# Kernel optimization log

Measured on AMD Instinct MI355X. Metric: run time of the kernel, lower is better.

Reference implementation:

```python
import jax, jax.numpy as jnp
import numpy as np

BN_EPS = 1e-5

def _conv(x, w, bias=None):
    # x: [N,C,H,W], w: [O,I,3,3], SAME padding, stride 1
    y = jax.lax.conv_general_dilated(x, w, window_strides=(1, 1),
                                     padding=((1, 1), (1, 1)),
                                     dimension_numbers=('NCHW', 'OIHW', 'NCHW'))
    if bias is not None:
        y = y + bias[None, :, None, None]
    return y

def _cconv(xr, xi, wr, wi):
    # complex conv: (xr + i xi) * (wr + i wi), cross-term combination
    return _conv(xr, wr) - _conv(xi, wi), _conv(xr, wi) + _conv(xi, wr)

def _bn1(x, g, b):
    # per-channel batchnorm (training-style stats over N,H,W)
    mu = jnp.mean(x, axis=(0, 2, 3), keepdims=True)
    var = jnp.var(x, axis=(0, 2, 3), keepdims=True)
    xh = (x - mu) * jax.lax.rsqrt(var + BN_EPS)
    return xh * g[None, :, None, None] + b[None, :, None, None]

def _cbn(xr, xi, g, b):
    # naive complex BN: normalize real/imag parts separately, shared affine
    return _bn1(xr, g, b), _bn1(xi, g, b)

def _crelu(xr, xi):
    return jax.nn.relu(xr), jax.nn.relu(xi)

def setup_inputs() -> dict:
    key = jax.random.key(0)
    ks = jax.random.split(key, 16)
    def w(k, o, i, kh=3, kw=3, s=0.05):
        return jax.random.normal(k, (o, i, kh, kw), jnp.float32) * s
    d = {}
    d['x'] = jax.random.normal(ks[0], (4, 256, 128, 224), jnp.float32)
    d['w1r'] = w(ks[1], 144, 256); d['w1i'] = w(ks[2], 144, 256)
    d['g1'] = jnp.ones((144,), jnp.float32); d['b1'] = jnp.zeros((144,), jnp.float32)
    d['w2r'] = w(ks[3], 96, 144); d['w2i'] = w(ks[4], 96, 144)
    d['g2'] = jnp.ones((96,), jnp.float32); d['b2'] = jnp.zeros((96,), jnp.float32)
    d['w3r'] = w(ks[5], 96, 96); d['w3i'] = w(ks[6], 96, 96)
    d['g3'] = jnp.ones((96,), jnp.float32); d['b3'] = jnp.zeros((96,), jnp.float32)
    d['w4r'] = w(ks[7], 96, 96); d['w4i'] = w(ks[8], 96, 96)
    d['g4'] = jnp.ones((96,), jnp.float32); d['b4'] = jnp.zeros((96,), jnp.float32)
    d['wc'] = w(ks[9], 1, 96); d['bc'] = jnp.zeros((1,), jnp.float32)
    d['wg'] = w(ks[10], 2, 96); d['bg'] = jnp.zeros((2,), jnp.float32)
    return d

def reference(x, w1r, w1i, g1, b1, w2r, w2i, g2, b2,
              w3r, w3i, g3, b3, w4r, w4i, g4, b4, wc, bc, wg, bg):
    # real input promoted to complex with zero imag
    xr, xi = x, jnp.zeros_like(x)
    xr, xi = _cconv(xr, xi, w1r, w1i)
    xr, xi = _cbn(xr, xi, g1, b1)
    xr, xi = _crelu(xr, xi)
    xr, xi = _cconv(xr, xi, w2r, w2i)
    xr, xi = _cbn(xr, xi, g2, b2)
    xr, xi = _crelu(xr, xi)
    xr, xi = _cconv(xr, xi, w3r, w3i)
    xr, xi = _cbn(xr, xi, g3, b3)
    xr, xi = _crelu(xr, xi)
    xr, xi = _cconv(xr, xi, w4r, w4i)
    xr, xi = _cbn(xr, xi, g4, b4)
    xr, xi = _crelu(xr, xi)
    x_mag = jnp.sqrt(xr * xr + xi * xi)  # torch.abs on complex
    cls = jax.nn.sigmoid(_conv(x_mag, wc, bc))
    reg = _conv(x_mag, wg, bg)
    return jnp.concatenate([cls, reg], axis=1)  # [N, 1+reg_layer, H, W]
```

## Files before the change

kernel.cpp:

```cpp
#include <hip/hip_runtime.h>
#include <cstdint>
#include <cstddef>

#define P_TOT 114688
#define W_IMG 224
#define H_IMG 128
#define WP 228
#define HP 130

typedef _Float16 f16;
typedef __attribute__((ext_vector_type(8))) _Float16 f16x8;
typedef __attribute__((ext_vector_type(4))) _Float16 f16x4;
typedef __attribute__((ext_vector_type(4))) float f32x4;

#define WAITVM(N) asm volatile("s_waitcnt vmcnt(" #N ")" ::: "memory")

__device__ __forceinline__ void barrier_sync() {
  asm volatile("" ::: "memory");
  __builtin_amdgcn_s_barrier();
  asm volatile("" ::: "memory");
}

__device__ __forceinline__ void gload16(const void* g, void* l) {
  __builtin_amdgcn_global_load_lds((const __attribute__((address_space(1))) void*)g,
                                   (__attribute__((address_space(3))) void*)l, 16, 0, 0);
}

__device__ __forceinline__ size_t pad_px(int n, int h, int w) {
  return ((size_t)(n * HP + h + 1)) * WP + (w + 1);
}

__global__ void k_halo(f16* __restrict__ slab, int CS) {
  int c8n = CS >> 3;
  int tid = blockIdx.x * 256 + threadIdx.x;
  int c8 = tid % c8n;
  int rest = tid / c8n;
  if (rest >= 4 * 968) return;
  int n = rest / 968, i = rest % 968;
  int h, w;
  if (i < 456) { h = (i < 228) ? 0 : 129; w = i % 228; }
  else { int j = i - 456; h = 1 + (j >> 2); int k = j & 3; w = (k == 0) ? 0 : (224 + k); }
  size_t pp = ((size_t)(n * HP + h)) * WP + w;
  *(f16x8*)(slab + pp * CS + c8 * 8) = (f16x8){0, 0, 0, 0, 0, 0, 0, 0};
}

__global__ void k_pack_x(const float* __restrict__ x, f16* __restrict__ xb) {
  int tid = threadIdx.x;
  int pw  = tid & 15;
  int c8  = tid >> 4;
  int p   = blockIdx.x * 16 + pw;
  int w   = p % W_IMG;
  int h   = (p / W_IMG) % H_IMG;
  int n   = p / (H_IMG * W_IMG);
  const float* src = x + ((size_t)(n * 256 + c8 * 8) * H_IMG + h) * W_IMG + w;
  f16x8 v;
#pragma unroll
  for (int j = 0; j < 8; j++) v[j] = (f16)src[(size_t)j * (H_IMG * W_IMG)];
  int c8s = (c8 & ~3) | ((c8 ^ (w >> 1)) & 3);
  *(f16x8*)(xb + pad_px(n, h, w) * 256 + c8s * 8) = v;
}

__global__ void k_pack_w(const float* __restrict__ wa, const float* __restrict__ wb,
                         f16* __restrict__ dst, int mode, int OT, int CS,
                         int Coh, int Cih, int total) {
  int gid = blockIdx.x * 256 + threadIdx.x;
  if (gid >= total) return;
  int j  = gid & 31;
  int t1 = gid >> 5;
  int o  = t1 % OT;
  int t2 = t1 / OT;
  int CCc = CS >> 5;
  int cc = t2 % CCc;
  int kk = t2 / CCc;
  int chunkT = ((j >> 3) ^ (o >> 1)) & 3;
  int is = cc * 32 + chunkT * 8 + (j & 7);
  float val = 0.f;
  if (mode == 0) {
    val = (o < Coh) ? wa[((size_t)o * Cih + is) * 9 + kk]
                    : wb[((size_t)(o - Coh) * Cih + is) * 9 + kk];
  } else if (mode == 1) {
    if (o < Coh) {
      val = (is < Cih) ? wa[((size_t)o * Cih + is) * 9 + kk]
                       : -wb[((size_t)o * Cih + (is - Cih)) * 9 + kk];
    } else {
      int oo = o - Coh;
      val = (is < Cih) ? wb[((size_t)oo * Cih + is) * 9 + kk]
                       : wa[((size_t)oo * Cih + (is - Cih)) * 9 + kk];
    }
  } else {
    if (o == 0)      val = wa[(size_t)is * 9 + kk];
    else if (o == 1) val = wb[(size_t)is * 9 + kk];
    else if (o == 2) val = wb[(size_t)(96 + is) * 9 + kk];
  }
  dst[gid] = (f16)val;
}

template<int BM, int OT, int CS, int WM, int WN, bool HEAD>
__launch_bounds__(WM * WN * 64)
__global__ void k_gemm(const f16* __restrict__ xb, const f16* __restrict__ Apack,
                       f16* __restrict__ y, float* __restrict__ outh,
                       const float* __restrict__ bcp, const float* __restrict__ bgp,
                       float* __restrict__ sums, float* __restrict__ sumsq) {
  constexpr int NT = WM * WN * 64;
  constexpr int NWV = NT / 64;
  constexpr int CC = CS / 32;
  constexpr int MF = BM / (WM * 16);
  constexpr int NF = 224 / (WN * 16);
  constexpr int NCH = 9 * CC;
  constexpr int TILE1 = (BM + 224) * 32;
  constexpr int ACH = BM / 16;
  constexpr int TCH = ACH + 14;
  constexpr int NHALF = HEAD ? 1 : 2;
  static_assert(HEAD || (TCH % NWV == 0 && TCH / NWV == 5), "vmcnt math: 5 loads/thread/half");
  __shared__ f16 lds[2][NHALF * TILE1];

  constexpr int NOT = OT / BM;
  constexpr int nwg = NOT * 512;
  int bid = blockIdx.x;
  int swz = (bid & 7) * (nwg >> 3) + (bid >> 3);
  const int ot = swz % NOT;
  const int rq = swz / NOT;
  const int n = rq >> 7;
  const int h = rq & 127;
  const int tid  = threadIdx.x;
  const int lane = tid & 63;
  const int wv   = tid >> 6;
  const int wm   = wv % WM;
  const int wn   = wv / WM;
  const int obase  = wm * (MF * 16);
  const int wnbase = wn * (NF * 16);
  const int l15 = lane & 15;
  const int lhi = lane >> 4;
  const int aoff = l15 * 64 + (((lhi ^ (l15 >> 1)) & 3) << 4);

  f32x4 acc[MF][NF];
#pragma unroll
  for (int mi = 0; mi < MF; mi++)
#pragma unroll
    for (int ni = 0; ni < NF; ni++) acc[mi][ni] = (f32x4){0.f, 0.f, 0.f, 0.f};

  const char* abase = (const char*)Apack + (size_t)ot * BM * 64 + lane * 16;
  const char* bbase = (const char*)xb +
      (pad_px(n, h, 0) + (lane >> 2)) * (CS * 2) + (lane & 3) * 16;

  auto stage1 = [&](char* base, int q) {
    const int kk = q / CC, c = q % CC;
    const int dh = kk / 3 - 1;
    const int dw = kk % 3 - 1;
    const char* asrc = abase + (size_t)q * (OT * 64);
    const char* bsrc = bbase + (dh * WP + dw) * (int)(CS * 2) + c * 64;
#pragma unroll
    for (int ck = wv; ck < TCH; ck += NWV) {
      char* dst = base + ck * 1024;
      if (ck < ACH) gload16(asrc + ck * 1024, dst);
      else          gload16(bsrc + (size_t)(ck - ACH) * (16 * CS * 2), dst);
    }
  };

  auto compute_half = [&](const char* base, int kk) {
    const int dw = kk % 3 - 1;
    const char* Ab = base;
    const char* Bb = base + BM * 64;
    f16x8 af[MF], bfr[NF];
#pragma unroll
    for (int mi = 0; mi < MF; mi++)
      af[mi] = *(const f16x8*)(Ab + (obase + mi * 16) * 64 + aoff);
#pragma unroll
    for (int ni = 0; ni < NF; ni++) {
      int px = wnbase + ni * 16 + l15;
      int sw = ((lhi ^ ((px + dw) >> 1)) & 3) << 4;
      bfr[ni] = *(const f16x8*)(Bb + px * 64 + sw);
    }
    __builtin_amdgcn_s_setprio(1);
#pragma unroll
    for (int mi = 0; mi < MF; mi++)
#pragma unroll
      for (int ni = 0; ni < NF; ni++)
        acc[mi][ni] = __builtin_amdgcn_mfma_f32_16x16x32_f16(af[mi], bfr[ni], acc[mi][ni], 0, 0, 0);
    __builtin_amdgcn_s_setprio(0);
  };

  if constexpr (!HEAD) {
    constexpr int STEPS = (NCH + 1) / 2;
    auto stage_pair = [&](int buf, int q) {
      char* b = (char*)&lds[buf][0];
      int q1 = (q + 1 < NCH) ? (q + 1) : (NCH - 1);
      stage1(b, q);
      stage1(b + TILE1 * 2, q1);
    };
    stage_pair(0, 0);
    for (int s = 0; s < STEPS; ++s) {
      int qn = (s + 1) * 2;
      if (qn < NCH) { stage_pair((s + 1) & 1, qn); WAITVM(10); }
      else          { WAITVM(0); }
      barrier_sync();
      const char* b = (const char*)&lds[s & 1][0];
      int q = s * 2;
      compute_half(b, q / CC);
      if (q + 1 < NCH) compute_half(b + TILE1 * 2, (q + 1) / CC);
      barrier_sync();
    }
  } else {
    stage1((char*)&lds[0][0], 0);
    __syncthreads();
    int buf = 0;
    for (int t = 0; t < NCH; ++t) {
      int tn = t + 1;
      if (tn < NCH) stage1((char*)&lds[buf ^ 1][0], tn);
      compute_half((const char*)&lds[buf][0], t / CC);
      __syncthreads();
      buf ^= 1;
    }
  }

  if constexpr (!HEAD) {
    const size_t prow = pad_px(n, h, 0);
#pragma unroll
    for (int mi = 0; mi < MF; mi++) {
#pragma unroll
      for (int ni = 0; ni < NF; ni++) {
        int o = obase + mi * 16 + lhi * 4;
        int w = wnbase + ni * 16 + l15;
        f16x4 v4;
#pragma unroll
        for (int j = 0; j < 4; j++) v4[j] = (f16)acc[mi][ni][j];
        *(f16x4*)(y + (prow + w) * OT + ot * BM + o) = v4;
      }
    }
    float sv[MF][4], qv[MF][4];
#pragma unroll
    for (int mi = 0; mi < MF; mi++)
#pragma unroll
      for (int j = 0; j < 4; j++) {
        float s = 0.f, q = 0.f;
#pragma unroll
        for (int ni = 0; ni < NF; ni++) {
          float v = acc[mi][ni][j];
          s += v; q += v * v;
        }
        sv[mi][j] = s; qv[mi][j] = q;
      }
#pragma unroll
    for (int m = 1; m < 16; m <<= 1) {
#pragma unroll
      for (int mi = 0; mi < MF; mi++)
#pragma unroll
        for (int j = 0; j < 4; j++) {
          sv[mi][j] += __shfl_xor(sv[mi][j], m);
          qv[mi][j] += __shfl_xor(qv[mi][j], m);
        }
    }
    if (l15 == 0) {
#pragma unroll
      for (int mi = 0; mi < MF; mi++)
#pragma unroll
        for (int j = 0; j < 4; j++) {
          int ch = ot * BM + obase + mi * 16 + lhi * 4 + j;
          atomicAdd(&sums[ch], sv[mi][j]);
          atomicAdd(&sumsq[ch], qv[mi][j]);
        }
    }
  } else {
    if (lhi == 0) {
      float b0 = bcp[0], b1 = bgp[0], b2 = bgp[1];
#pragma unroll
      for (int ni = 0; ni < NF; ni++) {
        int w = wnbase + ni * 16 + l15;
        float c0 = acc[0][ni][0] + b0;
        c0 = 1.f / (1.f + expf(-c0));
        float c1 = acc[0][ni][1] + b1;
        float c2 = acc[0][ni][2] + b2;
        outh[((size_t)(n * 3 + 0) * H_IMG + h) * W_IMG + w] = c0;
        outh[((size_t)(n * 3 + 1) * H_IMG + h) * W_IMG + w] = c1;
        outh[((size_t)(n * 3 + 2) * H_IMG + h) * W_IMG + w] = c2;
      }
    }
  }
}

template<int O>
__device__ __forceinline__ void bn_coef(const float* __restrict__ sums,
                                        const float* __restrict__ sumsq,
                                        const float* __restrict__ g,
                                        const float* __restrict__ b,
                                        float* sc, float* sh, int tid, int nt) {
  const float inv = 1.0f / (float)P_TOT;
  for (int t = tid; t < O; t += nt) {
    float mean = sums[t] * inv;
    float var  = fmaxf(sumsq[t] * inv - mean * mean, 0.f);
    int gi = (t < O / 2) ? t : (t - O / 2);
    float s = g[gi] * rsqrtf(var + 1e-5f);
    sc[t] = s;
    sh[t] = b[gi] - mean * s;
  }
}

template<int O>
__global__ void k_packip(f16* __restrict__ y,
                         const float* __restrict__ sums, const float* __restrict__ sumsq,
                         const float* __restrict__ g, const float* __restrict__ b) {
  __shared__ float sc[O], sh[O];
  bn_coef<O>(sums, sumsq, g, b, sc, sh, threadIdx.x, 256);
  __syncthreads();
  constexpr int G32 = O / 32;
  int gid = blockIdx.x * 256 + threadIdx.x;
  if (gid >= P_TOT * G32) return;
  int gg = gid % G32;
  int p = gid / G32;
  int w = p % W_IMG;
  int hh = (p / W_IMG) % H_IMG;
  int nn = p / (W_IMG * H_IMG);
  f16* base = y + pad_px(nn, hh, w) * O + gg * 32;
  f16x8 in[4];
#pragma unroll
  for (int ch = 0; ch < 4; ch++) in[ch] = *(const f16x8*)(base + ch * 8);
  int sw = (w >> 1) & 3;
  f16x8 outv[4];
#pragma unroll
  for (int ch = 0; ch < 4; ch++) {
#pragma unroll
    for (int j = 0; j < 8; j++) {
      int cdx = gg * 32 + ch * 8 + j;
      float f = fmaxf(fmaf((float)in[ch][j], sc[cdx], sh[cdx]), 0.f);
      outv[ch][j] = (f16)f;
    }
  }
#pragma unroll
  for (int ch = 0; ch < 4; ch++) *(f16x8*)(base + ((ch ^ sw) & 3) * 8) = outv[ch];
}

__global__ void k_mag(const f16* __restrict__ y,
                      const float* __restrict__ sums, const float* __restrict__ sumsq,
                      const float* __restrict__ g, const float* __restrict__ b,
                      f16* __restrict__ mg) {
  __shared__ float sc[192], sh[192];
  bn_coef<192>(sums, sumsq, g, b, sc, sh, threadIdx.x, 256);
  __syncthreads();
  int gid = blockIdx.x * 256 + threadIdx.x;
  if (gid >= P_TOT * 12) return;
  int c8 = gid % 12;
  int p  = gid / 12;
  int w  = p % W_IMG;
  int hh = (p / W_IMG) % H_IMG;
  int nn = p / (W_IMG * H_IMG);
  size_t pp = pad_px(nn, hh, w);
  f16x8 r8 = *(const f16x8*)(y + pp * 192 + c8 * 8);
  f16x8 i8 = *(const f16x8*)(y + pp * 192 + 96 + c8 * 8);
  f16x8 outv;
#pragma unroll
  for (int j = 0; j < 8; j++) {
    int cdx = c8 * 8 + j;
    float rr = fmaxf(fmaf((float)r8[j], sc[cdx], sh[cdx]), 0.f);
    float ii = fmaxf(fmaf((float)i8[j], sc[96 + cdx], sh[96 + cdx]), 0.f);
    outv[j] = (f16)sqrtf(rr * rr + ii * ii);
  }
  int c8s = (c8 & ~3) | ((c8 ^ (w >> 1)) & 3);
  *(f16x8*)(mg + pp * 96 + c8s * 8) = outv;
}

extern "C" void kernel_launch(void* const* d_in, const int* in_sizes, int n_in,
                              void* d_out, int out_size, void* d_ws, size_t ws_size,
                              hipStream_t stream) {
  const float* x   = (const float*)d_in[0];
  const float* w1r = (const float*)d_in[1];
  const float* w1i = (const float*)d_in[2];
  const float* g1  = (const float*)d_in[3];
  const float* b1  = (const float*)d_in[4];
  const float* w2r = (const float*)d_in[5];
  const float* w2i = (const float*)d_in[6];
  const float* g2  = (const float*)d_in[7];
  const float* b2  = (const float*)d_in[8];
  const float* w3r = (const float*)d_in[9];
  const float* w3i = (const float*)d_in[10];
  const float* g3  = (const float*)d_in[11];
  const float* b3  = (const float*)d_in[12];
  const float* w4r = (const float*)d_in[13];
  const float* w4i = (const float*)d_in[14];
  const float* g4  = (const float*)d_in[15];
  const float* b4  = (const float*)d_in[16];
  const float* wc  = (const float*)d_in[17];
  const float* bcp = (const float*)d_in[18];
  const float* wg  = (const float*)d_in[19];
  const float* bgp = (const float*)d_in[20];
  float* out = (float*)d_out;

  char* ws = (char*)d_ws;
  if (ws_size < 137500000ULL) return;

  auto S  = [&](int L) { return (float*)(ws + 16384 + L * 4096); };
  auto Q  = [&](int L) { return (float*)(ws + 16384 + L * 4096) + 512; };
  f16* A1 = (f16*)(ws + 65536);
  f16* A2 = (f16*)(ws + 1392640);
  f16* A3 = (f16*)(ws + 2387968);
  f16* A4 = (f16*)(ws + 3051520);
  f16* AH = (f16*)(ws + 3715072);
  f16* SLA = (f16*)(ws + 4194304);
  f16* SLB = (f16*)(ws + 65011712);

  hipMemsetAsync(d_ws, 0, 49152, stream);

  auto halo_grid = [](int CS) { return (4 * 968 * (CS / 8) + 255) / 256; };

  k_halo<<<halo_grid(256), 256, 0, stream>>>(SLA, 256);
  k_pack_x<<<P_TOT / 16, 512, 0, stream>>>(x, SLA);
  k_pack_w<<<(663552 + 255) / 256, 256, 0, stream>>>(w1r, w1i, A1, 0, 288, 256, 144, 256, 663552);
  k_pack_w<<<(497664 + 255) / 256, 256, 0, stream>>>(w2r, w2i, A2, 1, 192, 288, 96, 144, 497664);
  k_pack_w<<<(331776 + 255) / 256, 256, 0, stream>>>(w3r, w3i, A3, 1, 192, 192, 96, 96, 331776);
  k_pack_w<<<(331776 + 255) / 256, 256, 0, stream>>>(w4r, w4i, A4, 1, 192, 192, 96, 96, 331776);
  k_pack_w<<<(13824 + 255) / 256, 256, 0, stream>>>(wc, wg, AH, 2, 16, 96, 0, 96, 13824);
  k_halo<<<halo_grid(288), 256, 0, stream>>>(SLB, 288);

  k_gemm<96, 288, 256, 2, 2, false><<<1536, 256, 0, stream>>>(SLA, A1, SLB, nullptr, nullptr, nullptr, S(0), Q(0));
  k_packip<288><<<P_TOT * 9 / 256, 256, 0, stream>>>(SLB, S(0), Q(0), g1, b1);
  k_halo<<<halo_grid(192), 256, 0, stream>>>(SLA, 192);

  k_gemm<96, 192, 288, 2, 2, false><<<1024, 256, 0, stream>>>(SLB, A2, SLA, nullptr, nullptr, nullptr, S(1), Q(1));
  k_packip<192><<<P_TOT * 6 / 256, 256, 0, stream>>>(SLA, S(1), Q(1), g2, b2);
  k_halo<<<halo_grid(192), 256, 0, stream>>>(SLB, 192);

  k_gemm<96, 192, 192, 2, 2, false><<<1024, 256, 0, stream>>>(SLA, A3, SLB, nullptr, nullptr, nullptr, S(2), Q(2));
  k_packip<192><<<P_TOT * 6 / 256, 256, 0, stream>>>(SLB, S(2), Q(2), g3, b3);

  k_gemm<96, 192, 192, 2, 2, false><<<1024, 256, 0, stream>>>(SLB, A4, SLA, nullptr, nullptr, nullptr, S(3), Q(3));
  k_halo<<<halo_grid(96), 256, 0, stream>>>(SLB, 96);

  k_mag<<<P_TOT * 12 / 256, 256, 0, stream>>>(SLA, S(3), Q(3), g4, b4, SLB);

  k_gemm<16, 16, 96, 1, 2, true><<<512, 128, 0, stream>>>(SLB, AH, nullptr, out, bcp, bgp, nullptr, nullptr);

  (void)in_sizes; (void)n_in; (void)out_size;
}
```

Measured before the change: 883.7 us.

## Tile conv GEMM over flat padded pixel blocks of 256 with 512-thread workgroups

The implicit-GEMM conv kernels now tile over contiguous 256-pixel spans of the padded image instead of single 224-wide rows, using 8 waves (2x4) per 512-thread workgroup. Staging drops from two chunks per barrier to one chunk per step. Because tiles now cover halo columns, the epilogue writes garbage into halo positions and masks them out of the BN statistics, so the halo-zeroing kernels are moved after the packing kernels. The LDS swizzle is re-keyed on the flat padded pixel index everywhere. The goal is fewer, larger tiles with better MFMA utilisation and B-operand reuse, at the cost of extra computation on halo pixels.

```diff
diff --git a/kernel.cpp b/kernel.cpp
--- a/kernel.cpp
+++ b/kernel.cpp
@@ -7,6 +7,9 @@
 #define H_IMG 128
 #define WP 228
 #define HP 130
+#define IMG_PX (HP * WP)
+#define VALID_PX (128 * WP)
+#define NBLK_IMG (VALID_PX / 256)
 
 typedef _Float16 f16;
 typedef __attribute__((ext_vector_type(8))) _Float16 f16x8;
@@ -56,8 +59,9 @@
   f16x8 v;
 #pragma unroll
   for (int j = 0; j < 8; j++) v[j] = (f16)src[(size_t)j * (H_IMG * W_IMG)];
-  int c8s = (c8 & ~3) | ((c8 ^ (w >> 1)) & 3);
-  *(f16x8*)(xb + pad_px(n, h, w) * 256 + c8s * 8) = v;
+  size_t pp = pad_px(n, h, w);
+  int c8s = (c8 & ~3) | ((c8 ^ (int)(pp >> 1)) & 3);
+  *(f16x8*)(xb + pp * 256 + c8s * 8) = v;
 }
 
 __global__ void k_pack_w(const float* __restrict__ wa, const float* __restrict__ wb,
@@ -95,33 +99,48 @@
   dst[gid] = (f16)val;
 }
 
-template<int BM, int OT, int CS, int WM, int WN, bool HEAD>
-__launch_bounds__(WM * WN * 64)
+template<int OT, int CS, bool HEAD>
+__launch_bounds__(HEAD ? 128 : 512)
 __global__ void k_gemm(const f16* __restrict__ xb, const f16* __restrict__ Apack,
                        f16* __restrict__ y, float* __restrict__ outh,
                        const float* __restrict__ bcp, const float* __restrict__ bgp,
                        float* __restrict__ sums, float* __restrict__ sumsq) {
-  constexpr int NT = WM * WN * 64;
-  constexpr int NWV = NT / 64;
-  constexpr int CC = CS / 32;
-  constexpr int MF = BM / (WM * 16);
-  constexpr int NF = 224 / (WN * 16);
+  constexpr int BM  = HEAD ? 16 : 96;
+  constexpr int BN  = HEAD ? 224 : 256;
+  constexpr int WM  = HEAD ? 1 : 2;
+  constexpr int WN  = HEAD ? 2 : 4;
+  constexpr int NWV = WM * WN;
+  constexpr int CC  = CS / 32;
   constexpr int NCH = 9 * CC;
-  constexpr int TILE1 = (BM + 224) * 32;
+  constexpr int MF  = BM / (WM * 16);
+  constexpr int NF  = BN / (WN * 16);
   constexpr int ACH = BM / 16;
-  constexpr int TCH = ACH + 14;
-  constexpr int NHALF = HEAD ? 1 : 2;
-  static_assert(HEAD || (TCH % NWV == 0 && TCH / NWV == 5), "vmcnt math: 5 loads/thread/half");
-  __shared__ f16 lds[2][NHALF * TILE1];
+  constexpr int APAD = HEAD ? ACH : 8;
+  constexpr int BCH = BN / 16;
+  constexpr int TCH = APAD + BCH;
+  constexpr int LDSB = TCH * 1024;
+  __shared__ __align__(16) char lds[2][LDSB];
 
   constexpr int NOT = OT / BM;
-  constexpr int nwg = NOT * 512;
-  int bid = blockIdx.x;
-  int swz = (bid & 7) * (nwg >> 3) + (bid >> 3);
-  const int ot = swz % NOT;
-  const int rq = swz / NOT;
-  const int n = rq >> 7;
-  const int h = rq & 127;
+  constexpr int nwg = HEAD ? 512 : NOT * 4 * NBLK_IMG;
+  const int bid = blockIdx.x;
+  const int swz = (bid & 7) * (nwg >> 3) + (bid >> 3);
+
+  int ot, n, h;
+  size_t PB;
+  if constexpr (HEAD) {
+    ot = 0;
+    n = swz >> 7; h = swz & 127;
+    PB = pad_px(n, h, 0);
+  } else {
+    ot = swz % NOT;
+    int r = swz / NOT;
+    n = r / NBLK_IMG;
+    int blk = r % NBLK_IMG;
+    PB = (size_t)n * IMG_PX + WP + blk * 256;
+    h = 0;
+  }
+
   const int tid  = threadIdx.x;
   const int lane = tid & 63;
   const int wv   = tid >> 6;
@@ -132,6 +151,7 @@
   const int l15 = lane & 15;
   const int lhi = lane >> 4;
   const int aoff = l15 * 64 + (((lhi ^ (l15 >> 1)) & 3) << 4);
+  const int pblb = (int)PB;
 
   f32x4 acc[MF][NF];
 #pragma unroll
@@ -140,27 +160,37 @@
     for (int ni = 0; ni < NF; ni++) acc[mi][ni] = (f32x4){0.f, 0.f, 0.f, 0.f};
 
   const char* abase = (const char*)Apack + (size_t)ot * BM * 64 + lane * 16;
-  const char* bbase = (const char*)xb +
-      (pad_px(n, h, 0) + (lane >> 2)) * (CS * 2) + (lane & 3) * 16;
+  const char* bbase = (const char*)xb + (PB + (lane >> 2)) * (size_t)(CS * 2) + (lane & 3) * 16;
 
   auto stage1 = [&](char* base, int q) {
     const int kk = q / CC, c = q % CC;
-    const int dh = kk / 3 - 1;
-    const int dw = kk % 3 - 1;
+    const int doff = (kk / 3 - 1) * WP + (kk % 3 - 1);
     const char* asrc = abase + (size_t)q * (OT * 64);
-    const char* bsrc = bbase + (dh * WP + dw) * (int)(CS * 2) + c * 64;
-#pragma unroll
-    for (int ck = wv; ck < TCH; ck += NWV) {
-      char* dst = base + ck * 1024;
-      if (ck < ACH) gload16(asrc + ck * 1024, dst);
-      else          gload16(bsrc + (size_t)(ck - ACH) * (16 * CS * 2), dst);
+    const char* bsrc = bbase + doff * (CS * 2) + c * 64;
+    if constexpr (!HEAD) {
+#pragma unroll
+      for (int i = 0; i < TCH / NWV; i++) {
+        int ck = wv + i * NWV;
+        char* dst = base + ck * 1024;
+        const char* src = (ck < APAD) ? (asrc + ck * 1024)
+                                      : (bsrc + (ck - APAD) * (16 * CS * 2));
+        gload16(src, dst);
+      }
+    } else {
+      for (int ck = wv; ck < TCH; ck += NWV) {
+        char* dst = base + ck * 1024;
+        const char* src = (ck < APAD) ? (asrc + ck * 1024)
+                                      : (bsrc + (ck - APAD) * (16 * CS * 2));
+        gload16(src, dst);
+      }
     }
   };
 
-  auto compute_half = [&](const char* base, int kk) {
-    const int dw = kk % 3 - 1;
+  auto compute_half = [&](const char* base, int q) {
+    const int kk = q / CC;
+    const int pbl = pblb + (kk / 3 - 1) * WP + (kk % 3 - 1);
     const char* Ab = base;
-    const char* Bb = base + BM * 64;
+    const char* Bb = base + APAD * 1024;
     f16x8 af[MF], bfr[NF];
 #pragma unroll
     for (int mi = 0; mi < MF; mi++)
@@ -168,7 +198,7 @@
 #pragma unroll
     for (int ni = 0; ni < NF; ni++) {
       int px = wnbase + ni * 16 + l15;
-      int sw = ((lhi ^ ((px + dw) >> 1)) & 3) << 4;
+      int sw = ((lhi ^ ((pbl + px) >> 1)) & 3) << 4;
       bfr[ni] = *(const f16x8*)(Bb + px * 64 + sw);
     }
     __builtin_amdgcn_s_setprio(1);
@@ -181,51 +211,46 @@
   };
 
   if constexpr (!HEAD) {
-    constexpr int STEPS = (NCH + 1) / 2;
-    auto stage_pair = [&](int buf, int q) {
-      char* b = (char*)&lds[buf][0];
-      int q1 = (q + 1 < NCH) ? (q + 1) : (NCH - 1);
-      stage1(b, q);
-      stage1(b + TILE1 * 2, q1);
-    };
-    stage_pair(0, 0);
-    for (int s = 0; s < STEPS; ++s) {
-      int qn = (s + 1) * 2;
-      if (qn < NCH) { stage_pair((s + 1) & 1, qn); WAITVM(10); }
-      else          { WAITVM(0); }
+    stage1((char*)&lds[0][0], 0);
+    int buf = 0;
+    for (int t = 0; t < NCH; ++t) {
+      if (t + 1 < NCH) { stage1((char*)&lds[buf ^ 1][0], t + 1); WAITVM(3); }
+      else             { WAITVM(0); }
       barrier_sync();
-      const char* b = (const char*)&lds[s & 1][0];
-      int q = s * 2;
-      compute_half(b, q / CC);
-      if (q + 1 < NCH) compute_half(b + TILE1 * 2, (q + 1) / CC);
+      compute_half((const char*)&lds[buf][0], t);
       barrier_sync();
+      buf ^= 1;
     }
   } else {
     stage1((char*)&lds[0][0], 0);
     __syncthreads();
     int buf = 0;
     for (int t = 0; t < NCH; ++t) {
-      int tn = t + 1;
-      if (tn < NCH) stage1((char*)&lds[buf ^ 1][0], tn);
-      compute_half((const char*)&lds[buf][0], t / CC);
+      if (t + 1 < NCH) stage1((char*)&lds[buf ^ 1][0], t + 1);
+      compute_half((const char*)&lds[buf][0], t);
       __syncthreads();
       buf ^= 1;
     }
   }
 
   if constexpr (!HEAD) {
-    const size_t prow = pad_px(n, h, 0);
 #pragma unroll
     for (int mi = 0; mi < MF; mi++) {
 #pragma unroll
       for (int ni = 0; ni < NF; ni++) {
         int o = obase + mi * 16 + lhi * 4;
-        int w = wnbase + ni * 16 + l15;
+        int px = wnbase + ni * 16 + l15;
         f16x4 v4;
 #pragma unroll
         for (int j = 0; j < 4; j++) v4[j] = (f16)acc[mi][ni][j];
-        *(f16x4*)(y + (prow + w) * OT + ot * BM + o) = v4;
+        *(f16x4*)(y + (PB + px) * OT + ot * BM + o) = v4;
       }
+    }
+    float msk[NF];
+#pragma unroll
+    for (int ni = 0; ni < NF; ni++) {
+      int wcol = (int)((PB + (size_t)(wnbase + ni * 16 + l15)) % (size_t)WP);
+      msk[ni] = (wcol >= 1 && wcol <= 224) ? 1.f : 0.f;
     }
     float sv[MF][4], qv[MF][4];
 #pragma unroll
@@ -235,8 +260,8 @@
         float s = 0.f, q = 0.f;
 #pragma unroll
         for (int ni = 0; ni < NF; ni++) {
-          float v = acc[mi][ni][j];
-          s += v; q += v * v;
+          float v = acc[mi][ni][j] * msk[ni];
+          s += v; q += v * acc[mi][ni][j];
         }
         sv[mi][j] = s; qv[mi][j] = q;
       }
@@ -310,11 +335,12 @@
   int w = p % W_IMG;
   int hh = (p / W_IMG) % H_IMG;
   int nn = p / (W_IMG * H_IMG);
-  f16* base = y + pad_px(nn, hh, w) * O + gg * 32;
+  size_t pp = pad_px(nn, hh, w);
+  f16* base = y + pp * O + gg * 32;
   f16x8 in[4];
 #pragma unroll
   for (int ch = 0; ch < 4; ch++) in[ch] = *(const f16x8*)(base + ch * 8);
-  int sw = (w >> 1) & 3;
+  int sw = (int)(pp >> 1) & 3;
   f16x8 outv[4];
 #pragma unroll
   for (int ch = 0; ch < 4; ch++) {
@@ -354,7 +380,7 @@
     float ii = fmaxf(fmaf((float)i8[j], sc[96 + cdx], sh[96 + cdx]), 0.f);
     outv[j] = (f16)sqrtf(rr * rr + ii * ii);
   }
-  int c8s = (c8 & ~3) | ((c8 ^ (w >> 1)) & 3);
+  int c8s = (c8 & ~3) | ((c8 ^ (int)(pp >> 1)) & 3);
   *(f16x8*)(mg + pp * 96 + c8s * 8) = outv;
 }
 
@@ -390,12 +416,12 @@
   auto S  = [&](int L) { return (float*)(ws + 16384 + L * 4096); };
   auto Q  = [&](int L) { return (float*)(ws + 16384 + L * 4096) + 512; };
   f16* A1 = (f16*)(ws + 65536);
-  f16* A2 = (f16*)(ws + 1392640);
-  f16* A3 = (f16*)(ws + 2387968);
-  f16* A4 = (f16*)(ws + 3051520);
-  f16* AH = (f16*)(ws + 3715072);
-  f16* SLA = (f16*)(ws + 4194304);
-  f16* SLB = (f16*)(ws + 65011712);
+  f16* A2 = (f16*)(ws + 1441792);
+  f16* A3 = (f16*)(ws + 2490368);
+  f16* A4 = (f16*)(ws + 3211264);
+  f16* AH = (f16*)(ws + 3932160);
+  f16* SLA = (f16*)(ws + 5242880);
+  f16* SLB = (f16*)(ws + 67108864);
 
   hipMemsetAsync(d_ws, 0, 49152, stream);
 
@@ -408,25 +434,25 @@
   k_pack_w<<<(331776 + 255) / 256, 256, 0, stream>>>(w3r, w3i, A3, 1, 192, 192, 96, 96, 331776);
   k_pack_w<<<(331776 + 255) / 256, 256, 0, stream>>>(w4r, w4i, A4, 1, 192, 192, 96, 96, 331776);
   k_pack_w<<<(13824 + 255) / 256, 256, 0, stream>>>(wc, wg, AH, 2, 16, 96, 0, 96, 13824);
+
+  k_gemm<288, 256, false><<<3 * 4 * NBLK_IMG, 512, 0, stream>>>(SLA, A1, SLB, nullptr, nullptr, nullptr, S(0), Q(0));
+  k_packip<288><<<P_TOT * 9 / 256, 256, 0, stream>>>(SLB, S(0), Q(0), g1, b1);
   k_halo<<<halo_grid(288), 256, 0, stream>>>(SLB, 288);
 
-  k_gemm<96, 288, 256, 2, 2, false><<<1536, 256, 0, stream>>>(SLA, A1, SLB, nullptr, nullptr, nullptr, S(0), Q(0));
-  k_packip<288><<<P_TOT * 9 / 256, 256, 0, stream>>>(SLB, S(0), Q(0), g1, b1);
+  k_gemm<192, 288, false><<<2 * 4 * NBLK_IMG, 512, 0, stream>>>(SLB, A2, SLA, nullptr, nullptr, nullptr, S(1), Q(1));
+  k_packip<192><<<P_TOT * 6 / 256, 256, 0, stream>>>(SLA, S(1), Q(1), g2, b2);
   k_halo<<<halo_grid(192), 256, 0, stream>>>(SLA, 192);
 
-  k_gemm<96, 192, 288, 2, 2, false><<<1024, 256, 0, stream>>>(SLB, A2, SLA, nullptr, nullptr, nullptr, S(1), Q(1));
-  k_packip<192><<<P_TOT * 6 / 256, 256, 0, stream>>>(SLA, S(1), Q(1), g2, b2);
+  k_gemm<192, 192, false><<<2 * 4 * NBLK_IMG, 512, 0, stream>>>(SLA, A3, SLB, nullptr, nullptr, nullptr, S(2), Q(2));
+  k_packip<192><<<P_TOT * 6 / 256, 256, 0, stream>>>(SLB, S(2), Q(2), g3, b3);
   k_halo<<<halo_grid(192), 256, 0, stream>>>(SLB, 192);
 
-  k_gemm<96, 192, 192, 2, 2, false><<<1024, 256, 0, stream>>>(SLA, A3, SLB, nullptr, nullptr, nullptr, S(2), Q(2));
-  k_packip<192><<<P_TOT * 6 / 256, 256, 0, stream>>>(SLB, S(2), Q(2), g3, b3);
-
-  k_gemm<96, 192, 192, 2, 2, false><<<1024, 256, 0, stream>>>(SLB, A4, SLA, nullptr, nullptr, nullptr, S(3), Q(3));
+  k_gemm<192, 192, false><<<2 * 4 * NBLK_IMG, 512, 0, stream>>>(SLB, A4, SLA, nullptr, nullptr, nullptr, S(3), Q(3));
+
+  k_mag<<<P_TOT * 12 / 256, 256, 0, stream>>>(SLA, S(3), Q(3), g4, b4, SLB);
   k_halo<<<halo_grid(96), 256, 0, stream>>>(SLB, 96);
 
-  k_mag<<<P_TOT * 12 / 256, 256, 0, stream>>>(SLA, S(3), Q(3), g4, b4, SLB);
-
-  k_gemm<16, 16, 96, 1, 2, true><<<512, 128, 0, stream>>>(SLB, AH, nullptr, out, bcp, bgp, nullptr, nullptr);
+  k_gemm<16, 96, true><<<512, 128, 0, stream>>>(SLB, AH, nullptr, out, bcp, bgp, nullptr, nullptr);
 
   (void)in_sizes; (void)n_in; (void)out_size;
 }
```

Result: slower. 1.198 ms (+35.5%).

## Triple-buffer LDS stages and prefetch register fragments ahead of MFMA

Applied to the files above, without the earlier changes.

Replaces the double-buffered two-chunks-per-step loop with a three-buffer ring of single K-chunks. Fragments for the next chunk are read from LDS into a second register set while MFMAs run on the current set, and sched_group_barrier hints ask the compiler to interleave the LDS reads with the MFMAs. The goal is to hide LDS read latency and the global load wait behind matrix math. It also requests two workgroups per CU via launch_bounds, which may cap register use, and the extra fragment registers raise register pressure and could cause spills.

```diff
diff --git a/kernel.cpp b/kernel.cpp
--- a/kernel.cpp
+++ b/kernel.cpp
@@ -96,7 +96,7 @@
 }
 
 template<int BM, int OT, int CS, int WM, int WN, bool HEAD>
-__launch_bounds__(WM * WN * 64)
+__launch_bounds__(WM * WN * 64, HEAD ? 1 : 2)
 __global__ void k_gemm(const f16* __restrict__ xb, const f16* __restrict__ Apack,
                        f16* __restrict__ y, float* __restrict__ outh,
                        const float* __restrict__ bcp, const float* __restrict__ bgp,
@@ -110,9 +110,9 @@
   constexpr int TILE1 = (BM + 224) * 32;
   constexpr int ACH = BM / 16;
   constexpr int TCH = ACH + 14;
-  constexpr int NHALF = HEAD ? 1 : 2;
-  static_assert(HEAD || (TCH % NWV == 0 && TCH / NWV == 5), "vmcnt math: 5 loads/thread/half");
-  __shared__ f16 lds[2][NHALF * TILE1];
+  constexpr int NBUF = HEAD ? 2 : 3;
+  static_assert(HEAD || (TCH % NWV == 0 && TCH / NWV == 5), "vmcnt math: 5 loads/thread/stage");
+  __shared__ __align__(16) f16 lds[NBUF][TILE1];
 
   constexpr int NOT = OT / BM;
   constexpr int nwg = NOT * 512;
@@ -141,14 +141,13 @@
 
   const char* abase = (const char*)Apack + (size_t)ot * BM * 64 + lane * 16;
   const char* bbase = (const char*)xb +
-      (pad_px(n, h, 0) + (lane >> 2)) * (CS * 2) + (lane & 3) * 16;
+      (pad_px(n, h, 0) + (lane >> 2)) * (size_t)(CS * 2) + (lane & 3) * 16;
 
   auto stage1 = [&](char* base, int q) {
     const int kk = q / CC, c = q % CC;
-    const int dh = kk / 3 - 1;
-    const int dw = kk % 3 - 1;
+    const int doff = (kk / 3 - 1) * WP + (kk % 3 - 1);
     const char* asrc = abase + (size_t)q * (OT * 64);
-    const char* bsrc = bbase + (dh * WP + dw) * (int)(CS * 2) + c * 64;
+    const char* bsrc = bbase + doff * (CS * 2) + c * 64;
 #pragma unroll
     for (int ck = wv; ck < TCH; ck += NWV) {
       char* dst = base + ck * 1024;
@@ -157,11 +156,10 @@
     }
   };
 
-  auto compute_half = [&](const char* base, int kk) {
-    const int dw = kk % 3 - 1;
+  auto read_frags = [&](const char* base, int q, f16x8* af, f16x8* bfr) {
+    const int dw = (q / CC) % 3 - 1;
     const char* Ab = base;
     const char* Bb = base + BM * 64;
-    f16x8 af[MF], bfr[NF];
 #pragma unroll
     for (int mi = 0; mi < MF; mi++)
       af[mi] = *(const f16x8*)(Ab + (obase + mi * 16) * 64 + aoff);
@@ -171,6 +169,9 @@
       int sw = ((lhi ^ ((px + dw) >> 1)) & 3) << 4;
       bfr[ni] = *(const f16x8*)(Bb + px * 64 + sw);
     }
+  };
+
+  auto mfma21 = [&](const f16x8* af, const f16x8* bfr) {
     __builtin_amdgcn_s_setprio(1);
 #pragma unroll
     for (int mi = 0; mi < MF; mi++)
@@ -181,40 +182,52 @@
   };
 
   if constexpr (!HEAD) {
-    constexpr int STEPS = (NCH + 1) / 2;
-    auto stage_pair = [&](int buf, int q) {
-      char* b = (char*)&lds[buf][0];
-      int q1 = (q + 1 < NCH) ? (q + 1) : (NCH - 1);
-      stage1(b, q);
-      stage1(b + TILE1 * 2, q1);
-    };
-    stage_pair(0, 0);
-    for (int s = 0; s < STEPS; ++s) {
-      int qn = (s + 1) * 2;
-      if (qn < NCH) { stage_pair((s + 1) & 1, qn); WAITVM(10); }
-      else          { WAITVM(0); }
-      barrier_sync();
-      const char* b = (const char*)&lds[s & 1][0];
-      int q = s * 2;
-      compute_half(b, q / CC);
-      if (q + 1 < NCH) compute_half(b + TILE1 * 2, (q + 1) / CC);
-      barrier_sync();
+    f16x8 afA[MF], bfA[NF], afB[MF], bfB[NF];
+    stage1((char*)&lds[0][0], 0);
+    stage1((char*)&lds[1][0], 1);
+    WAITVM(5);
+    barrier_sync();
+    read_frags((const char*)&lds[0][0], 0, afA, bfA);
+    for (int t = 0; t < NCH; t += 2) {
+      if (t + 2 < NCH) { stage1((char*)&lds[(t + 2) % 3][0], t + 2); WAITVM(5); }
+      else if (t + 1 < NCH) { WAITVM(0); }
+      if (t + 1 < NCH) {
+        barrier_sync();
+        read_frags((const char*)&lds[(t + 1) % 3][0], t + 1, afB, bfB);
+        __builtin_amdgcn_sched_group_barrier(0x100, MF + NF, 0);
+        __builtin_amdgcn_sched_group_barrier(0x008, MF * NF, 0);
+      }
+      mfma21(afA, bfA);
+      if (t + 1 < NCH) barrier_sync();
+      if (t + 1 < NCH) {
+        if (t + 3 < NCH) { stage1((char*)&lds[(t + 3) % 3][0], t + 3); WAITVM(5); }
+        else if (t + 2 < NCH) { WAITVM(0); }
+        if (t + 2 < NCH) {
+          barrier_sync();
+          read_frags((const char*)&lds[(t + 2) % 3][0], t + 2, afA, bfA);
+          __builtin_amdgcn_sched_group_barrier(0x100, MF + NF, 0);
+          __builtin_amdgcn_sched_group_barrier(0x008, MF * NF, 0);
+        }
+        mfma21(afB, bfB);
+        if (t + 2 < NCH) barrier_sync();
+      }
     }
   } else {
+    f16x8 afA[MF], bfA[NF];
     stage1((char*)&lds[0][0], 0);
     __syncthreads();
     int buf = 0;
     for (int t = 0; t < NCH; ++t) {
-      int tn = t + 1;
-      if (tn < NCH) stage1((char*)&lds[buf ^ 1][0], tn);
-      compute_half((const char*)&lds[buf][0], t / CC);
+      if (t + 1 < NCH) stage1((char*)&lds[buf ^ 1][0], t + 1);
+      read_frags((const char*)&lds[buf][0], t, afA, bfA);
+      mfma21(afA, bfA);
       __syncthreads();
       buf ^= 1;
     }
   }
 
+  const size_t prow = pad_px(n, h, 0);
   if constexpr (!HEAD) {
-    const size_t prow = pad_px(n, h, 0);
 #pragma unroll
     for (int mi = 0; mi < MF; mi++) {
 #pragma unroll
```

Result: slower. 1.468 ms (+66.1%).

## Stage per-wave private LDS tiles to remove workgroup barriers in conv GEMM

Applied to the files above, without the earlier changes.

The non-head GEMM path now has each wave load its own A and B fragments into a private double-buffered LDS region and wait only on its own vmcnt and lgkmcnt. This replaces the shared tile and the two workgroup barriers per step. The aim is to remove barrier stalls and let waves run out of lockstep. The cost is that A and B data shared between waves is loaded redundantly, which raises global/L2 traffic and LDS footprint and may lower occupancy.

```diff
diff --git a/kernel.cpp b/kernel.cpp
--- a/kernel.cpp
+++ b/kernel.cpp
@@ -14,12 +14,7 @@
 typedef __attribute__((ext_vector_type(4))) float f32x4;
 
 #define WAITVM(N) asm volatile("s_waitcnt vmcnt(" #N ")" ::: "memory")
-
-__device__ __forceinline__ void barrier_sync() {
-  asm volatile("" ::: "memory");
-  __builtin_amdgcn_s_barrier();
-  asm volatile("" ::: "memory");
-}
+#define WAITLGKM0() asm volatile("s_waitcnt lgkmcnt(0)" ::: "memory")
 
 __device__ __forceinline__ void gload16(const void* g, void* l) {
   __builtin_amdgcn_global_load_lds((const __attribute__((address_space(1))) void*)g,
@@ -107,12 +102,12 @@
   constexpr int MF = BM / (WM * 16);
   constexpr int NF = 224 / (WN * 16);
   constexpr int NCH = 9 * CC;
-  constexpr int TILE1 = (BM + 224) * 32;
-  constexpr int ACH = BM / 16;
-  constexpr int TCH = ACH + 14;
-  constexpr int NHALF = HEAD ? 1 : 2;
-  static_assert(HEAD || (TCH % NWV == 0 && TCH / NWV == 5), "vmcnt math: 5 loads/thread/half");
-  __shared__ f16 lds[2][NHALF * TILE1];
+  constexpr int AKB = MF;
+  constexpr int BKB = NF;
+  constexpr int WREG = (AKB + BKB) * 1024;
+  constexpr int LDS_BYTES = HEAD ? (2 * 15 * 1024) : (2 * NWV * WREG);
+  static_assert(HEAD || AKB + BKB == 10, "vmcnt(10) math: 10 loads/thread/stage");
+  __shared__ __align__(16) char lds[LDS_BYTES];
 
   constexpr int NOT = OT / BM;
   constexpr int nwg = NOT * 512;
@@ -131,7 +126,7 @@
   const int wnbase = wn * (NF * 16);
   const int l15 = lane & 15;
   const int lhi = lane >> 4;
-  const int aoff = l15 * 64 + (((lhi ^ (l15 >> 1)) & 3) << 4);
+  const int aslot = (((lhi ^ (l15 >> 1)) & 3) << 4);
 
   f32x4 acc[MF][NF];
 #pragma unroll
@@ -139,38 +134,11 @@
 #pragma unroll
     for (int ni = 0; ni < NF; ni++) acc[mi][ni] = (f32x4){0.f, 0.f, 0.f, 0.f};
 
-  const char* abase = (const char*)Apack + (size_t)ot * BM * 64 + lane * 16;
+  const char* abase = (const char*)Apack + ((size_t)ot * BM + (HEAD ? 0 : obase)) * 64 + lane * 16;
   const char* bbase = (const char*)xb +
-      (pad_px(n, h, 0) + (lane >> 2)) * (CS * 2) + (lane & 3) * 16;
-
-  auto stage1 = [&](char* base, int q) {
-    const int kk = q / CC, c = q % CC;
-    const int dh = kk / 3 - 1;
-    const int dw = kk % 3 - 1;
-    const char* asrc = abase + (size_t)q * (OT * 64);
-    const char* bsrc = bbase + (dh * WP + dw) * (int)(CS * 2) + c * 64;
-#pragma unroll
-    for (int ck = wv; ck < TCH; ck += NWV) {
-      char* dst = base + ck * 1024;
-      if (ck < ACH) gload16(asrc + ck * 1024, dst);
-      else          gload16(bsrc + (size_t)(ck - ACH) * (16 * CS * 2), dst);
-    }
-  };
-
-  auto compute_half = [&](const char* base, int kk) {
-    const int dw = kk % 3 - 1;
-    const char* Ab = base;
-    const char* Bb = base + BM * 64;
-    f16x8 af[MF], bfr[NF];
-#pragma unroll
-    for (int mi = 0; mi < MF; mi++)
-      af[mi] = *(const f16x8*)(Ab + (obase + mi * 16) * 64 + aoff);
-#pragma unroll
-    for (int ni = 0; ni < NF; ni++) {
-      int px = wnbase + ni * 16 + l15;
-      int sw = ((lhi ^ ((px + dw) >> 1)) & 3) << 4;
-      bfr[ni] = *(const f16x8*)(Bb + px * 64 + sw);
-    }
+      (pad_px(n, h, 0) + (HEAD ? 0 : wnbase) + (lane >> 2)) * (size_t)(CS * 2) + (lane & 3) * 16;
+
+  auto mfma_cluster = [&](const f16x8* af, const f16x8* bfr) {
     __builtin_amdgcn_s_setprio(1);
 #pragma unroll
     for (int mi = 0; mi < MF; mi++)
@@ -181,40 +149,84 @@
   };
 
   if constexpr (!HEAD) {
-    constexpr int STEPS = (NCH + 1) / 2;
-    auto stage_pair = [&](int buf, int q) {
-      char* b = (char*)&lds[buf][0];
-      int q1 = (q + 1 < NCH) ? (q + 1) : (NCH - 1);
-      stage1(b, q);
-      stage1(b + TILE1 * 2, q1);
+    auto stage_own = [&](char* wbase, int q) {
+      const int kk = q / CC, c = q % CC;
+      const int doff = (kk / 3 - 1) * WP + (kk % 3 - 1);
+      const char* asrc = abase + (size_t)q * (OT * 64);
+      const char* bsrc = bbase + (ptrdiff_t)doff * (CS * 2) + c * 64;
+#pragma unroll
+      for (int ck = 0; ck < AKB; ck++)
+        gload16(asrc + ck * 1024, wbase + ck * 1024);
+#pragma unroll
+      for (int ck = 0; ck < BKB; ck++)
+        gload16(bsrc + (size_t)ck * (16 * CS * 2), wbase + AKB * 1024 + ck * 1024);
     };
-    stage_pair(0, 0);
-    for (int s = 0; s < STEPS; ++s) {
-      int qn = (s + 1) * 2;
-      if (qn < NCH) { stage_pair((s + 1) & 1, qn); WAITVM(10); }
-      else          { WAITVM(0); }
-      barrier_sync();
-      const char* b = (const char*)&lds[s & 1][0];
-      int q = s * 2;
-      compute_half(b, q / CC);
-      if (q + 1 < NCH) compute_half(b + TILE1 * 2, (q + 1) / CC);
-      barrier_sync();
+    auto read_frags = [&](const char* wbase, int q, f16x8* af, f16x8* bfr) {
+      const int dw = (q / CC) % 3 - 1;
+#pragma unroll
+      for (int mi = 0; mi < MF; mi++)
+        af[mi] = *(const f16x8*)(wbase + (mi * 16 + l15) * 64 + aslot);
+#pragma unroll
+      for (int ni = 0; ni < NF; ni++) {
+        int px = wnbase + ni * 16 + l15;
+        int sw = ((lhi ^ ((px + dw) >> 1)) & 3) << 4;
+        bfr[ni] = *(const f16x8*)(wbase + AKB * 1024 + (ni * 16 + l15) * 64 + sw);
+      }
+    };
+    char* w0 = lds + wv * WREG;
+    char* w1 = lds + NWV * WREG + wv * WREG;
+    f16x8 af[MF], bfr[NF];
+    stage_own(w0, 0);
+    stage_own(w1, 1);
+    for (int t = 0; t < NCH; ++t) {
+      char* wb = (t & 1) ? w1 : w0;
+      if (t + 1 < NCH) { WAITVM(10); }
+      else             { WAITVM(0); }
+      read_frags(wb, t, af, bfr);
+      mfma_cluster(af, bfr);
+      __builtin_amdgcn_sched_barrier(0);
+      WAITLGKM0();
+      __builtin_amdgcn_sched_barrier(0);
+      if (t + 2 < NCH) stage_own(wb, t + 2);
     }
   } else {
-    stage1((char*)&lds[0][0], 0);
+    constexpr int TCH = 1 + 14;
+    auto stage_blk = [&](char* base, int q) {
+      const int kk = q / CC, c = q % CC;
+      const int doff = (kk / 3 - 1) * WP + (kk % 3 - 1);
+      const char* asrc = abase + (size_t)q * (OT * 64);
+      const char* bsrc = bbase + (ptrdiff_t)doff * (CS * 2) + c * 64;
+      for (int ck = wv; ck < TCH; ck += NWV) {
+        char* dst = base + ck * 1024;
+        if (ck < 1) gload16(asrc, dst);
+        else        gload16(bsrc + (size_t)(ck - 1) * (16 * CS * 2), dst);
+      }
+    };
+    auto read_frags_blk = [&](const char* base, int q, f16x8* af, f16x8* bfr) {
+      const int dw = (q / CC) % 3 - 1;
+      af[0] = *(const f16x8*)(base + l15 * 64 + aslot);
+#pragma unroll
+      for (int ni = 0; ni < NF; ni++) {
+        int px = wnbase + ni * 16 + l15;
+        int sw = ((lhi ^ ((px + dw) >> 1)) & 3) << 4;
+        bfr[ni] = *(const f16x8*)(base + 1024 + px * 64 + sw);
+      }
+    };
+    f16x8 af[MF], bfr[NF];
+    stage_blk(lds, 0);
     __syncthreads();
     int buf = 0;
     for (int t = 0; t < NCH; ++t) {
-      int tn = t + 1;
-      if (tn < NCH) stage1((char*)&lds[buf ^ 1][0], tn);
-      compute_half((const char*)&lds[buf][0], t / CC);
+      if (t + 1 < NCH) stage_blk(lds + (buf ^ 1) * 15360, t + 1);
+      read_frags_blk(lds + buf * 15360, t, af, bfr);
+      mfma_cluster(af, bfr);
       __syncthreads();
       buf ^= 1;
     }
   }
 
+  const size_t prow = pad_px(n, h, 0);
   if constexpr (!HEAD) {
-    const size_t prow = pad_px(n, h, 0);
 #pragma unroll
     for (int mi = 0; mi < MF; mi++) {
 #pragma unroll
```

Measured after the change: 1.009 ms. +14.2%, slower.
